# Kernel optimization log

Measured on AMD Instinct MI355X. Metric: run time of the kernel, lower is better.

## Reference

```python
import jax, jax.numpy as jnp
import numpy as np

T, N, H, L, V, B, MAX_NB = 32, 1024, 256, 128, 800, 256, 15
E = T * N  # total messages; buffer row E is the zero-pad slot


def setup_inputs() -> dict:
    key = jax.random.key(0)
    ks = jax.random.split(key, 12)

    def lin(k, o, i):
        return jax.random.normal(k, (o, i), jnp.float32) / np.float32(np.sqrt(i))

    rng = np.random.default_rng(0)
    # neighbor message indices: at step t only messages produced at steps < t are valid
    h_nei_idx = rng.integers(0, E, size=(T, N, MAX_NB))
    o_nei_idx = rng.integers(0, E, size=(T, N, MAX_NB))
    limit = (np.arange(T) * N)[:, None, None]
    h_nei_idx = np.where(h_nei_idx < limit, h_nei_idx, E)
    o_nei_idx = np.where(o_nei_idx < limit, o_nei_idx, E)

    return dict(
        emb=jax.random.normal(ks[0], (V, H), jnp.float32) * 0.02,
        W_z_w=lin(ks[1], H, 2 * H), W_z_b=jnp.zeros((H,), jnp.float32),
        W_r_w=lin(ks[2], H, H), W_r_b=jnp.zeros((H,), jnp.float32),
        U_r_w=lin(ks[3], H, H),
        W_h_w=lin(ks[4], H, 2 * H), W_h_b=jnp.zeros((H,), jnp.float32),
        W_w=lin(ks[5], H, H + L), W_b=jnp.zeros((H,), jnp.float32),
        Wo_w=lin(ks[6], V, H), Wo_b=jnp.zeros((V,), jnp.float32),
        U_w=lin(ks[7], H, H + L), U_b=jnp.zeros((H,), jnp.float32),
        Ui_w=lin(ks[8], H, 2 * H), Ui_b=jnp.zeros((H,), jnp.float32),
        Uo_w=lin(ks[9], 1, H), Uo_b=jnp.zeros((1,), jnp.float32),
        x_tree_vecs=jax.random.normal(ks[10], (B, L), jnp.float32),
        word_ids=jnp.asarray(rng.integers(0, V, size=(T, N)), jnp.int32),
        h_nei_idx=jnp.asarray(h_nei_idx, jnp.int32),
        o_nei_idx=jnp.asarray(o_nei_idx, jnp.int32),
        contexts=jnp.asarray(rng.integers(0, B, size=(T, N)), jnp.int32),
        pred_targets=jnp.asarray(rng.integers(0, V, size=(T, N)), jnp.int32),
        direction=jnp.asarray(rng.integers(0, 2, size=(T, N)), jnp.int32),
        root_word_ids=jnp.asarray(rng.integers(0, V, size=(B,)), jnp.int32),
        root_o_idx=jnp.asarray(rng.integers(0, E + 1, size=(B, MAX_NB)), jnp.int32),
    )


def reference(emb, W_z_w, W_z_b, W_r_w, W_r_b, U_r_w, W_h_w, W_h_b,
              W_w, W_b, Wo_w, Wo_b, U_w, U_b, Ui_w, Ui_b, Uo_w, Uo_b,
              x_tree_vecs, word_ids, h_nei_idx, o_nei_idx, contexts,
              pred_targets, direction, root_word_ids, root_o_idx):
    f32 = jnp.float32

    def gru(x, h_nei):  # x: [N,H], h_nei: [N,MAX_NB,H]
        sum_h = h_nei.sum(1)
        z = jax.nn.sigmoid(jnp.concatenate([x, sum_h], -1) @ W_z_w.T + W_z_b)
        r = jax.nn.sigmoid((x @ W_r_w.T + W_r_b)[:, None, :] + h_nei @ U_r_w.T)
        gated = (r * h_nei).sum(1)
        h_tilde = jnp.tanh(jnp.concatenate([x, gated], -1) @ W_h_w.T + W_h_b)
        return (1.0 - z) * sum_h + z * h_tilde

    def step(hbuf, xs):
        t, wid, hidx, oidx = xs
        x = emb[wid]                      # [N,H] embedding gather
        new_h = gru(x, hbuf[hidx])        # gather -> GRU
        cur_o = hbuf[oidx].sum(1)         # padded neighbor sum for stop head
        hbuf = jax.lax.dynamic_update_slice(hbuf, new_h, (t * N, 0))  # scatter
        return hbuf, (new_h, jnp.concatenate([x, cur_o], -1))

    hbuf0 = jnp.zeros((E + 1, H), f32)
    hbuf, (new_h_all, stop_h_all) = jax.lax.scan(
        step, hbuf0, (jnp.arange(T), word_ids, h_nei_idx, o_nei_idx))

    def aggregate(hid, ctx, Vw, Vb, Vow, Vob):
        iv = jnp.concatenate([hid, x_tree_vecs[ctx]], -1)
        return jax.nn.relu(iv @ Vw.T + Vb) @ Vow.T + Vob

    # ---- word prediction head: root entries (zero hidden) + direction==1 edges
    pred_hid = jnp.concatenate([jnp.zeros((B, H), f32), new_h_all.reshape(E, H)], 0)
    pred_ctx = jnp.concatenate([jnp.arange(B, dtype=jnp.int32), contexts.reshape(E)], 0)
    pred_tgt = jnp.concatenate([root_word_ids, pred_targets.reshape(E)], 0)
    pred_mask = jnp.concatenate([jnp.ones((B,), f32), direction.reshape(E).astype(f32)], 0)
    scores = aggregate(pred_hid, pred_ctx, W_w, W_b, Wo_w, Wo_b)  # [B+E, V]
    nll = -jnp.take_along_axis(jax.nn.log_softmax(scores, -1), pred_tgt[:, None], 1)[:, 0]
    pred_loss = (nll * pred_mask).sum() / B
    pred_acc = ((scores.argmax(-1) == pred_tgt).astype(f32) * pred_mask).sum() / pred_mask.sum()

    # ---- stop head: all edges + root closing entries
    root_stop = jnp.concatenate([emb[root_word_ids], hbuf[root_o_idx].sum(1)], -1)
    stop_hid = jnp.concatenate([stop_h_all.reshape(E, 2 * H), root_stop], 0)
    stop_ctx = jnp.concatenate([contexts.reshape(E), jnp.arange(B, dtype=jnp.int32)], 0)
    stop_tgt = jnp.concatenate([direction.reshape(E).astype(f32), jnp.zeros((B,), f32)], 0)
    stop_hid = jax.nn.relu(stop_hid @ Ui_w.T + Ui_b)  # U_i with relu
    s = aggregate(stop_hid, stop_ctx, U_w, U_b, Uo_w, Uo_b)[:, 0]
    bce = jnp.maximum(s, 0.0) - s * stop_tgt + jnp.log1p(jnp.exp(-jnp.abs(s)))
    stop_loss = bce.sum() / B
    stop_acc = ((s >= 0.0).astype(f32) == stop_tgt).astype(f32).mean()

    return pred_loss, stop_loss, pred_acc, stop_acc
```

## Files before the change

### kernel.cpp

```cpp
#include <hip/hip_runtime.h>
#include <math.h>


namespace {

constexpr int T_  = 32;
constexpr int N_  = 1024;
constexpr int H_  = 256;
constexpr int NB_ = 15;
constexpr int E_  = T_ * N_;
constexpr int B_  = 256;
constexpr int PREDB_ = (B_ + E_) / 64;
constexpr int STOPB_ = (E_ + B_) / 64;

typedef unsigned short u16;
typedef unsigned int   u32;
typedef unsigned int  uix4  __attribute__((ext_vector_type(4)));
typedef __bf16        bf16x8 __attribute__((ext_vector_type(8)));
typedef float         f32x4  __attribute__((ext_vector_type(4)));

__device__ __forceinline__ float sig_(float x){ return 1.f / (1.f + __expf(-x)); }

__device__ __forceinline__ float b2f(u16 u){
  union { u32 i; float f; } v; v.i = ((u32)u) << 16; return v.f;
}
__device__ __forceinline__ u16 f2b(float f){
  union { float f; u32 i; } v; v.f = f;
  const u32 r = v.i + 0x7fffu + ((v.i >> 16) & 1u);
  return (u16)(r >> 16);
}
__device__ __forceinline__ f32x4 mfma16(uix4 a, uix4 b, f32x4 c){
  return __builtin_amdgcn_mfma_f32_16x16x32_bf16(
      __builtin_bit_cast(bf16x8, a), __builtin_bit_cast(bf16x8, b), c, 0, 0, 0);
}

__global__ __launch_bounds__(256) void k_cvt(
    const float* __restrict__ emb, const float* __restrict__ xt,
    const float* __restrict__ Ww,  const float* __restrict__ Wo,
    const float* __restrict__ Ui,  const float* __restrict__ Uw,
    const float* __restrict__ Wz,  const float* __restrict__ Wr,
    const float* __restrict__ Ur,  const float* __restrict__ Wh,
    u16* __restrict__ o_emb, u16* __restrict__ o_xt, u16* __restrict__ o_Ww,
    u16* __restrict__ o_Wo,  u16* __restrict__ o_Ui, u16* __restrict__ o_Uw,
    u16* __restrict__ o_Wz,  u16* __restrict__ o_Wr, u16* __restrict__ o_Ur,
    u16* __restrict__ o_Wh)
{
  int i = blockIdx.x * 256 + threadIdx.x;
  if (i < 204800){ o_emb[i] = f2b(emb[i]); return; }  i -= 204800;
  if (i <  32768){ o_xt[i]  = f2b(xt[i]);  return; }  i -=  32768;
  if (i <  98304){ o_Ww[i]  = f2b(Ww[i]);  return; }  i -=  98304;
  if (i < 204800){ o_Wo[i]  = f2b(Wo[i]);  return; }  i -= 204800;
  if (i < 131072){ o_Ui[i]  = f2b(Ui[i]);  return; }  i -= 131072;
  if (i <  98304){ o_Uw[i]  = f2b(Uw[i]);  return; }  i -=  98304;
  if (i < 131072){ o_Wz[i]  = f2b(Wz[i]);  return; }  i -= 131072;
  if (i <  65536){ o_Wr[i]  = f2b(Wr[i]);  return; }  i -=  65536;
  if (i <  65536){ o_Ur[i]  = f2b(Ur[i]);  return; }  i -=  65536;
  if (i < 131072){ o_Wh[i]  = f2b(Wh[i]); }
}

__global__ __launch_bounds__(256) void k_rep(
    const u16* __restrict__ Ur16, const u16* __restrict__ Wz16,
    const u16* __restrict__ Wh16, const u16* __restrict__ Ui16,
    u16* __restrict__ UrF, u16* __restrict__ WzF, u16* __restrict__ WhF,
    u16* __restrict__ UiF)
{
  const int idx = blockIdx.x * 256 + threadIdx.x;
  if (idx < 24576){
    const int mat = idx >> 13, r = idx & 8191;
    const int ctkb = r >> 6, lane = r & 63;
    const int ct = ctkb >> 3, kb = ctkb & 7;
    const int q = lane >> 4, m = lane & 15;
    const int col = ct * 16 + m;
    const u16* src;
    u16* dst;
    if (mat == 0){ src = Ur16 + (size_t)col*256 +       kb*32 + q*8; dst = UrF; }
    else if (mat == 1){ src = Wz16 + (size_t)col*512 + 256 + kb*32 + q*8; dst = WzF; }
    else { src = Wh16 + (size_t)col*512 + 256 + kb*32 + q*8; dst = WhF; }
    *(uix4*)(dst + (size_t)r * 8) = *(const uix4*)src;
  } else {
    const int r = idx - 24576;
    if (r >= 16384) return;
    const int ctkb = r >> 6, lane = r & 63;
    const int ct = ctkb >> 4, kb = ctkb & 15;
    const int q = lane >> 4, m = lane & 15;
    const int col = ct * 16 + m;
    *(uix4*)(UiF + (size_t)r * 8) =
        *(const uix4*)(Ui16 + (size_t)col*512 + kb*32 + q*8);
  }
}

__global__ __launch_bounds__(256) void k_init(float* __restrict__ acc,
                                              u16* __restrict__ hb16){
  const int tid = threadIdx.x;
  if (tid < 16) acc[tid] = 0.f;
  hb16[(size_t)E_ * H_ + tid] = 0;
}

__global__ __launch_bounds__(256) void k_tab(
    const u16* __restrict__ emb16,
    const u16* __restrict__ Wr16, const float* __restrict__ Wrb,
    const u16* __restrict__ Wz16, const float* __restrict__ Wzb,
    const u16* __restrict__ Wh16, const float* __restrict__ Whb,
    float* __restrict__ xrtab, float* __restrict__ xztab,
    float* __restrict__ xhtab)
{
  const int tid = threadIdx.x;
  const int w = tid >> 6, ln = tid & 63, q = ln >> 4, m = ln & 15;
  const int r0 = blockIdx.x * 16;

  uix4 Ae[8];
  {
    const u16* ep = emb16 + (size_t)(r0 + m) * 256 + q * 8;
    #pragma unroll
    for (int kb = 0; kb < 8; ++kb) Ae[kb] = *(const uix4*)(ep + kb * 32);
  }
  #pragma unroll
  for (int nt = 0; nt < 4; ++nt){
    const int col = w * 64 + nt * 16 + m;
    f32x4 ar = {0.f,0.f,0.f,0.f}, az = {0.f,0.f,0.f,0.f}, ah = {0.f,0.f,0.f,0.f};
    const u16* br = Wr16 + (size_t)col * 256 + q * 8;
    const u16* bz = Wz16 + (size_t)col * 512 + q * 8;
    const u16* bh = Wh16 + (size_t)col * 512 + q * 8;
    #pragma unroll
    for (int kb = 0; kb < 8; ++kb){
      ar = mfma16(Ae[kb], *(const uix4*)(br + kb*32), ar);
      az = mfma16(Ae[kb], *(const uix4*)(bz + kb*32), az);
      ah = mfma16(Ae[kb], *(const uix4*)(bh + kb*32), ah);
    }
    const float rb = Wrb[col], zb = Wzb[col], hb = Whb[col];
    #pragma unroll
    for (int i = 0; i < 4; ++i){
      const size_t o = (size_t)(r0 + 4*q + i) * 256 + col;
      xrtab[o] = ar[i] + rb;
      xztab[o] = az[i] + zb;
      xhtab[o] = ah[i] + hb;
    }
  }
}

__global__ __launch_bounds__(1024, 4) void k_gru(
    const u16* __restrict__ UrF, const u16* __restrict__ WzF,
    const u16* __restrict__ WhF,
    const float* __restrict__ xrtab, const float* __restrict__ xztab,
    const float* __restrict__ xhtab,
    const int* __restrict__ word_ids, const int* __restrict__ h_nei,
    u16* __restrict__ hb16, int t)
{
  __shared__ __align__(16) u16 hn[64 * 264];
  __shared__ __align__(16) u16 sh[4][264];
  __shared__ __align__(16) u16 gl[4][264];
  __shared__ int s_wid[4];
  __shared__ int s_hidx[64];

  const int tid = threadIdx.x;
  const int w = tid >> 6, ln = tid & 63, q = ln >> 4, m = ln & 15;
  const int col  = w * 16 + m;
  const int base = t * N_ + blockIdx.x * 4;

  if (tid < 4) s_wid[tid] = word_ids[base + tid];
  if (tid < 64){
    const int row = tid & 3, nb = tid >> 2;
    s_hidx[tid] = (nb < NB_) ? h_nei[(base + row) * NB_ + nb] : E_;
  }

  const u16* urb = UrF + (size_t)(w * 8) * 512 + ln * 8;
  uix4 b0 = *(const uix4*)(urb);
  uix4 b1 = *(const uix4*)(urb + 512);
  uix4 b2 = *(const uix4*)(urb + 1024);
  uix4 b3 = *(const uix4*)(urb + 1536);
  uix4 b4 = *(const uix4*)(urb + 2048);
  uix4 b5 = *(const uix4*)(urb + 2560);
  uix4 b6 = *(const uix4*)(urb + 3072);
  uix4 b7 = *(const uix4*)(urb + 3584);

  __syncthreads();

  #pragma unroll
  for (int it = 0; it < 2; ++it){
    const int task = it * 1024 + tid;
    const int row = task >> 5, ch = task & 31;
    *(uix4*)(&hn[row*264 + ch*8]) =
        *(const uix4*)(hb16 + (size_t)s_hidx[row]*256 + ch*8);
  }
  __syncthreads();

  f32x4 xr;
  #pragma unroll
  for (int i = 0; i < 4; ++i) xr[i] = xrtab[(size_t)s_wid[i] * 256 + col];

  float ga[4] = {0.f,0.f,0.f,0.f}, su[4] = {0.f,0.f,0.f,0.f};
  #pragma unroll
  for (int j = 0; j < 4; ++j){
    uix4 Ah[8];
    #pragma unroll
    for (int kb = 0; kb < 8; ++kb)
      Ah[kb] = *(const uix4*)(&hn[(j*16 + m)*264 + kb*32 + q*8]);
    f32x4 a = xr;
    a = mfma16(Ah[0], b0, a); a = mfma16(Ah[1], b1, a);
    a = mfma16(Ah[2], b2, a); a = mfma16(Ah[3], b3, a);
    a = mfma16(Ah[4], b4, a); a = mfma16(Ah[5], b5, a);
    a = mfma16(Ah[6], b6, a); a = mfma16(Ah[7], b7, a);
    #pragma unroll
    for (int i = 0; i < 4; ++i){
      const float hv = b2f(hn[(j*16 + 4*q + i)*264 + col]);
      ga[i] += sig_(a[i]) * hv;
      su[i] += hv;
    }
  }

  #pragma unroll
  for (int i = 0; i < 4; ++i){
    ga[i] += __shfl_xor(ga[i], 16, 64);
    ga[i] += __shfl_xor(ga[i], 32, 64);
    su[i] += __shfl_xor(su[i], 16, 64);
    su[i] += __shfl_xor(su[i], 32, 64);
  }
  if (q == 0){
    #pragma unroll
    for (int i = 0; i < 4; ++i){
      sh[i][col] = f2b(su[i]);
      gl[i][col] = f2b(ga[i]);
    }
  }
  __syncthreads();

  f32x4 az, ah;
  #pragma unroll
  for (int i = 0; i < 4; ++i){
    az[i] = xztab[(size_t)s_wid[i] * 256 + col];
    ah[i] = xhtab[(size_t)s_wid[i] * 256 + col];
  }
  {
    const u16* zb = WzF + (size_t)(w * 8) * 512 + ln * 8;
    uix4 Bz[8];
    #pragma unroll
    for (int kb = 0; kb < 8; ++kb) Bz[kb] = *(const uix4*)(zb + kb * 512);
    uix4 As[8];
    #pragma unroll
    for (int kb = 0; kb < 8; ++kb) As[kb] = *(const uix4*)(&sh[m & 3][kb*32 + q*8]);
    #pragma unroll
    for (int kb = 0; kb < 8; ++kb) az = mfma16(As[kb], Bz[kb], az);
  }
  {
    const u16* hb = WhF + (size_t)(w * 8) * 512 + ln * 8;
    uix4 Bh[8];
    #pragma unroll
    for (int kb = 0; kb < 8; ++kb) Bh[kb] = *(const uix4*)(hb + kb * 512);
    uix4 Ag[8];
    #pragma unroll
    for (int kb = 0; kb < 8; ++kb) Ag[kb] = *(const uix4*)(&gl[m & 3][kb*32 + q*8]);
    #pragma unroll
    for (int kb = 0; kb < 8; ++kb) ah = mfma16(Ag[kb], Bh[kb], ah);
  }
  if (q == 0){
    #pragma unroll
    for (int i = 0; i < 4; ++i){
      const float z  = sig_(az[i]);
      const float ht = tanhf(ah[i]);
      const float nh = (1.f - z) * su[i] + z * ht;
      hb16[(size_t)(base + i) * 256 + col] = f2b(nh);
    }
  }
}

struct PredSm {
  u16   hd[4][16][264];
  u16   bt[32 * 264];
  int   tgt[64];
  float mask[64];
  float nll[64], hit[64], msk[64];
};
struct StopSm {
  u16   so[64][264];
  u16   bt[16 * 392];
  int   oidx[64][NB_];
  int   wid[64], ctx[64];
  float tgt[64];
  float b0[64], b1[64];
};
constexpr size_t SMU_ = sizeof(StopSm) > sizeof(PredSm) ? sizeof(StopSm)
                                                        : sizeof(PredSm);

__device__ void pred_body(int bid, char* smraw,
    const u16* __restrict__ hb16, const u16* __restrict__ Ww16,
    const float* __restrict__ Wb, const u16* __restrict__ Wo16,
    const float* __restrict__ Wob, const u16* __restrict__ xt16,
    const int* __restrict__ contexts, const int* __restrict__ pred_targets,
    const int* __restrict__ direction, const int* __restrict__ root_word_ids,
    float* __restrict__ accum)
{
  PredSm& sm = *(PredSm*)smraw;
  const int tid = threadIdx.x;
  const int p0  = bid * 64;
  const int w = tid >> 6, ln = tid & 63, q = ln >> 4, m = ln & 15;
  const int r0 = w * 16;

  if (tid < 64){
    const int p = p0 + tid;
    int tg; float mk;
    if (p < B_){ tg = root_word_ids[p]; mk = 1.f; }
    else { tg = pred_targets[p - B_]; mk = (float)direction[p - B_]; }
    sm.tgt[tid] = tg; sm.mask[tid] = mk;
  }
  const int p    = p0 + r0 + m;
  const int hrow = (p < B_) ? E_ : (p - B_);
  const int ctx  = (p < B_) ? p  : contexts[p - B_];

  uix4 A1[12];
  {
    const u16* hp = hb16 + (size_t)hrow * 256 + q * 8;
    #pragma unroll
    for (int j = 0; j < 8; ++j) A1[j] = *(const uix4*)(hp + j * 32);
    const u16* xp = xt16 + (size_t)ctx * 128 + q * 8;
    #pragma unroll
    for (int j = 0; j < 4; ++j) A1[8 + j] = *(const uix4*)(xp + j * 32);
  }

  {
    #pragma unroll
    for (int j = 0; j < 3; ++j){
      const int i = j*256 + tid, r = i / 48, c = i % 48;
      *(uix4*)(&sm.bt[r*392 + c*8]) = *(const uix4*)(Ww16 + (size_t)i*8);
    }
  }
  __syncthreads();
  for (int t = 0; t < 16; ++t){
    uix4 pf[3];
    if (t < 15){
      const u16* src = Ww16 + (size_t)(t+1)*16*384;
      #pragma unroll
      for (int j = 0; j < 3; ++j)
        pf[j] = *(const uix4*)(src + (size_t)(j*256 + tid)*8);
    }
    f32x4 acc = {0.f, 0.f, 0.f, 0.f};
    const u16* bp = &sm.bt[m*392 + q*8];
    #pragma unroll
    for (int j = 0; j < 12; ++j) acc = mfma16(A1[j], *(const uix4*)(bp + j*32), acc);
    const float bias = Wb[t*16 + m];
    #pragma unroll
    for (int i = 0; i < 4; ++i)
      sm.hd[w][q*4 + i][t*16 + m] = f2b(fmaxf(acc[i] + bias, 0.f));
    __syncthreads();
    if (t < 15){
      #pragma unroll
      for (int j = 0; j < 3; ++j){
        const int i = j*256 + tid, r = i / 48, c = i % 48;
        *(uix4*)(&sm.bt[r*392 + c*8]) = pf[j];
      }
      __syncthreads();
    }
  }

  uix4 A2[8];
  #pragma unroll
  for (int j = 0; j < 8; ++j) A2[j] = *(const uix4*)(&sm.hd[w][m][j*32 + q*8]);

  int tgtc[4];
  #pragma unroll
  for (int i = 0; i < 4; ++i) tgtc[i] = sm.tgt[r0 + q*4 + i];
  float lrun[4], amax[4], tval[4]; int aidx[4];
  #pragma unroll
  for (int i = 0; i < 4; ++i){
    lrun[i] = 0.f; amax[i] = -1e30f; tval[i] = -1e30f; aidx[i] = 0;
  }

  {
    #pragma unroll
    for (int j = 0; j < 4; ++j){
      const int i = j*256 + tid, r = i >> 5, c = i & 31;
      *(uix4*)(&sm.bt[r*264 + c*8]) = *(const uix4*)(Wo16 + (size_t)i*8);
    }
  }
  __syncthreads();
  for (int pp = 0; pp < 25; ++pp){
    uix4 pf[4];
    if (pp < 24){
      const u16* src = Wo16 + (size_t)(pp+1)*32*256;
      #pragma unroll
      for (int j = 0; j < 4; ++j)
        pf[j] = *(const uix4*)(src + (size_t)(j*256 + tid)*8);
    }
    f32x4 a0 = {0.f,0.f,0.f,0.f}, a1 = {0.f,0.f,0.f,0.f};
    const u16* bp0 = &sm.bt[m*264 + q*8];
    const u16* bp1 = &sm.bt[(16 + m)*264 + q*8];
    #pragma unroll
    for (int j = 0; j < 8; ++j){
      a0 = mfma16(A2[j], *(const uix4*)(bp0 + j*32), a0);
      a1 = mfma16(A2[j], *(const uix4*)(bp1 + j*32), a1);
    }
    const int c0 = pp*32 + m, c1 = c0 + 16;
    const float bias0 = Wob[c0], bias1 = Wob[c1];
    #pragma unroll
    for (int i = 0; i < 4; ++i){
      const float v0 = a0[i] + bias0;
      const float v1 = a1[i] + bias1;
      if (c0 == tgtc[i]) tval[i] = v0;
      if (c1 == tgtc[i]) tval[i] = v1;
      if (v0 > amax[i]){ amax[i] = v0; aidx[i] = c0; }
      if (v1 > amax[i]){ amax[i] = v1; aidx[i] = c1; }
      lrun[i] += __expf(v0) + __expf(v1);
    }
    __syncthreads();
    if (pp < 24){
      #pragma unroll
      for (int j = 0; j < 4; ++j){
        const int i = j*256 + tid, r = i >> 5, cc = i & 31;
        *(uix4*)(&sm.bt[r*264 + cc*8]) = pf[j];
      }
      __syncthreads();
    }
  }
  #pragma unroll
  for (int msk = 1; msk < 16; msk <<= 1){
    #pragma unroll
    for (int i = 0; i < 4; ++i){
      lrun[i] += __shfl_xor(lrun[i], msk, 64);
      const float oa = __shfl_xor(amax[i], msk, 64);
      const int   oi = __shfl_xor(aidx[i], msk, 64);
      if (oa > amax[i] || (oa == amax[i] && oi < aidx[i])){ amax[i] = oa; aidx[i] = oi; }
      tval[i] = fmaxf(tval[i], __shfl_xor(tval[i], msk, 64));
    }
  }
  if (m == 0){
    #pragma unroll
    for (int i = 0; i < 4; ++i){
      const int r = r0 + q*4 + i;
      const float mk  = sm.mask[r];
      const float nll = __logf(lrun[i]) - tval[i];
      sm.nll[r] = nll * mk;
      sm.hit[r] = (aidx[i] == tgtc[i]) ? mk : 0.f;
      sm.msk[r] = mk;
    }
  }
  __syncthreads();
  if (tid < 64){
    float a = sm.nll[tid], b = sm.hit[tid], c2 = sm.msk[tid];
    #pragma unroll
    for (int off = 32; off > 0; off >>= 1){
      a += __shfl_down(a, off, 64); b += __shfl_down(b, off, 64); c2 += __shfl_down(c2, off, 64);
    }
    if (tid == 0){
      atomicAdd(&accum[0], a); atomicAdd(&accum[1], b); atomicAdd(&accum[2], c2);
    }
  }
}

__device__ void stop_body(int bid, char* smraw,
    const u16* __restrict__ hb16, const u16* __restrict__ emb16,
    const u16* __restrict__ UiF,  const float* __restrict__ Uib,
    const u16* __restrict__ Uw16, const float* __restrict__ Ub,
    const float* __restrict__ Uo, const float* __restrict__ Uob,
    const u16* __restrict__ xt16,
    const int* __restrict__ word_ids, const int* __restrict__ o_nei,
    const int* __restrict__ contexts, const int* __restrict__ direction,
    const int* __restrict__ root_word_ids, const int* __restrict__ root_o_idx,
    float* __restrict__ accum)
{
  StopSm& sm = *(StopSm*)smraw;
  const int tid = threadIdx.x;
  const int p0  = bid * 64;
  const int w = tid >> 6, ln = tid & 63, q = ln >> 4, m = ln & 15;
  const int r0 = w * 16;

  if (tid < 64){
    const int s = p0 + tid;
    if (s < E_){ sm.wid[tid] = word_ids[s]; sm.ctx[tid] = contexts[s];
                 sm.tgt[tid] = (float)direction[s]; }
    else { const int b = s - E_; sm.wid[tid] = root_word_ids[b]; sm.ctx[tid] = b;
           sm.tgt[tid] = 0.f; }
  }
  for (int k = tid; k < 64 * NB_; k += 256){
    const int r = k / NB_, nb = k % NB_;
    const int s = p0 + r;
    sm.oidx[r][nb] = (s < E_) ? o_nei[(size_t)s * NB_ + nb]
                              : root_o_idx[(size_t)(s - E_) * NB_ + nb];
  }
  __syncthreads();

  for (int it = 0; it < 4; ++it){
    const int task = it * 256 + tid;
    const int row = task >> 4, sl = task & 15;
    float a[16];
    #pragma unroll
    for (int c = 0; c < 16; ++c) a[c] = 0.f;
    #pragma unroll
    for (int nb = 0; nb < NB_; ++nb){
      const u16* p = hb16 + (size_t)sm.oidx[row][nb] * 256 + sl * 16;
      const uix4 v0 = *(const uix4*)(p);
      const uix4 v1 = *(const uix4*)(p + 8);
      #pragma unroll
      for (int c = 0; c < 4; ++c){
        a[2*c]     += b2f((u16)(v0[c] & 0xffffu));
        a[2*c + 1] += b2f((u16)(v0[c] >> 16));
        a[8 + 2*c] += b2f((u16)(v1[c] & 0xffffu));
        a[9 + 2*c] += b2f((u16)(v1[c] >> 16));
      }
    }
    uix4 o0, o1;
    #pragma unroll
    for (int c = 0; c < 4; ++c){
      o0[c] = (u32)f2b(a[2*c])   | ((u32)f2b(a[2*c+1]) << 16);
      o1[c] = (u32)f2b(a[8+2*c]) | ((u32)f2b(a[9+2*c]) << 16);
    }
    *(uix4*)(&sm.so[row][sl*16])     = o0;
    *(uix4*)(&sm.so[row][sl*16 + 8]) = o1;
  }
  __syncthreads();

  uix4 A1[16];
  {
    const u16* ep = emb16 + (size_t)sm.wid[r0 + m] * 256 + q * 8;
    #pragma unroll
    for (int j = 0; j < 8; ++j) A1[j] = *(const uix4*)(ep + j * 32);
    #pragma unroll
    for (int j = 0; j < 8; ++j) A1[8 + j] = *(const uix4*)(&sm.so[r0 + m][j*32 + q*8]);
  }
  __syncthreads();

  for (int t = 0; t < 16; ++t){
    const u16* bp = UiF + (size_t)(t * 16) * 512 + ln * 8;
    uix4 Bf[16];
    #pragma unroll
    for (int kb = 0; kb < 16; ++kb) Bf[kb] = *(const uix4*)(bp + kb * 512);
    f32x4 acc = {0.f, 0.f, 0.f, 0.f};
    #pragma unroll
    for (int kb = 0; kb < 16; ++kb) acc = mfma16(A1[kb], Bf[kb], acc);
    const float bias = Uib[t*16 + m];
    #pragma unroll
    for (int i = 0; i < 4; ++i)
      sm.so[r0 + q*4 + i][t*16 + m] = f2b(fmaxf(acc[i] + bias, 0.f));
  }
  __syncthreads();

  uix4 A2[12];
  {
    #pragma unroll
    for (int j = 0; j < 8; ++j) A2[j] = *(const uix4*)(&sm.so[r0 + m][j*32 + q*8]);
    const u16* xp = xt16 + (size_t)sm.ctx[r0 + m] * 128 + q * 8;
    #pragma unroll
    for (int j = 0; j < 4; ++j) A2[8 + j] = *(const uix4*)(xp + j * 32);
  }
  float sp[4] = {0.f, 0.f, 0.f, 0.f};
  {
    #pragma unroll
    for (int j = 0; j < 3; ++j){
      const int i = j*256 + tid, r = i / 48, c = i % 48;
      *(uix4*)(&sm.bt[r*392 + c*8]) = *(const uix4*)(Uw16 + (size_t)i*8);
    }
  }
  __syncthreads();
  for (int t = 0; t < 16; ++t){
    uix4 pf[3];
    if (t < 15){
      const u16* src = Uw16 + (size_t)(t+1)*16*384;
      #pragma unroll
      for (int j = 0; j < 3; ++j)
        pf[j] = *(const uix4*)(src + (size_t)(j*256 + tid)*8);
    }
    f32x4 acc = {0.f, 0.f, 0.f, 0.f};
    const u16* bp = &sm.bt[m*392 + q*8];
    #pragma unroll
    for (int j = 0; j < 12; ++j) acc = mfma16(A2[j], *(const uix4*)(bp + j*32), acc);
    const int c = t*16 + m;
    const float bias = Ub[c];
    const float uo   = Uo[c];
    #pragma unroll
    for (int i = 0; i < 4; ++i) sp[i] += fmaxf(acc[i] + bias, 0.f) * uo;
    __syncthreads();
    if (t < 15){
      #pragma unroll
      for (int j = 0; j < 3; ++j){
        const int i = j*256 + tid, r = i / 48, cc = i % 48;
        *(uix4*)(&sm.bt[r*392 + cc*8]) = pf[j];
      }
      __syncthreads();
    }
  }
  #pragma unroll
  for (int msk = 1; msk < 16; msk <<= 1){
    #pragma unroll
    for (int i = 0; i < 4; ++i) sp[i] += __shfl_xor(sp[i], msk, 64);
  }
  if (m == 0){
    const float ub = Uob[0];
    #pragma unroll
    for (int i = 0; i < 4; ++i){
      const int r = r0 + q*4 + i;
      const float s   = sp[i] + ub;
      const float tgt = sm.tgt[r];
      sm.b0[r] = fmaxf(s, 0.f) - s * tgt + log1pf(__expf(-fabsf(s)));
      const float pb = (s >= 0.f) ? 1.f : 0.f;
      sm.b1[r] = (pb == tgt) ? 1.f : 0.f;
    }
  }
  __syncthreads();
  if (tid < 64){
    float a = sm.b0[tid], b = sm.b1[tid];
    #pragma unroll
    for (int off = 32; off > 0; off >>= 1){
      a += __shfl_down(a, off, 64); b += __shfl_down(b, off, 64);
    }
    if (tid == 0){ atomicAdd(&accum[3], a); atomicAdd(&accum[4], b); }
  }
}

__global__ __launch_bounds__(256, 3) void k_heads(
    const u16* __restrict__ hb16, const u16* __restrict__ emb16,
    const u16* __restrict__ Ww16, const float* __restrict__ Wb,
    const u16* __restrict__ Wo16, const float* __restrict__ Wob,
    const u16* __restrict__ UiF,  const float* __restrict__ Uib,
    const u16* __restrict__ Uw16, const float* __restrict__ Ub,
    const float* __restrict__ Uo, const float* __restrict__ Uob,
    const u16* __restrict__ xt16,
    const int* __restrict__ word_ids, const int* __restrict__ o_nei,
    const int* __restrict__ contexts, const int* __restrict__ pred_targets,
    const int* __restrict__ direction, const int* __restrict__ root_word_ids,
    const int* __restrict__ root_o_idx, float* __restrict__ accum)
{
  __shared__ __align__(16) char smraw[SMU_];
  const int b = blockIdx.x;
  if (b < PREDB_){
    pred_body(b, smraw, hb16, Ww16, Wb, Wo16, Wob, xt16,
              contexts, pred_targets, direction, root_word_ids, accum);
  } else {
    stop_body(b - PREDB_, smraw, hb16, emb16, UiF, Uib, Uw16, Ub, Uo, Uob,
              xt16, word_ids, o_nei, contexts, direction,
              root_word_ids, root_o_idx, accum);
  }
}

__global__ void k_final(const float* __restrict__ acc, float* __restrict__ out){
  if (threadIdx.x == 0 && blockIdx.x == 0){
    out[0] = acc[0] / (float)B_;
    out[1] = acc[3] / (float)B_;
    out[2] = acc[1] / acc[2];
    out[3] = acc[4] / (float)(E_ + B_);
  }
}

}

extern "C" void kernel_launch(void* const* d_in, const int* in_sizes, int n_in,
                              void* d_out, int out_size, void* d_ws, size_t ws_size,
                              hipStream_t stream)
{
  const float* emb   = (const float*)d_in[0];
  const float* Wz    = (const float*)d_in[1];
  const float* Wzb   = (const float*)d_in[2];
  const float* Wr    = (const float*)d_in[3];
  const float* Wrb   = (const float*)d_in[4];
  const float* Ur    = (const float*)d_in[5];
  const float* Wh    = (const float*)d_in[6];
  const float* Whb   = (const float*)d_in[7];
  const float* Ww    = (const float*)d_in[8];
  const float* Wb    = (const float*)d_in[9];
  const float* Wo    = (const float*)d_in[10];
  const float* Wob   = (const float*)d_in[11];
  const float* Uw    = (const float*)d_in[12];
  const float* Ub    = (const float*)d_in[13];
  const float* Ui    = (const float*)d_in[14];
  const float* Uib   = (const float*)d_in[15];
  const float* Uo    = (const float*)d_in[16];
  const float* Uob   = (const float*)d_in[17];
  const float* xtree = (const float*)d_in[18];
  const int* word_ids      = (const int*)d_in[19];
  const int* h_nei_idx     = (const int*)d_in[20];
  const int* o_nei_idx     = (const int*)d_in[21];
  const int* contexts      = (const int*)d_in[22];
  const int* pred_targets  = (const int*)d_in[23];
  const int* direction     = (const int*)d_in[24];
  const int* root_word_ids = (const int*)d_in[25];
  const int* root_o_idx    = (const int*)d_in[26];

  char*  wsb   = (char*)d_ws;
  float* accum = (float*)wsb;
  size_t off = 256 + 4096;
  u16* hb16  = (u16*)(wsb + off); off += (size_t)(E_ + 1) * H_ * 2;
  u16* emb16 = (u16*)(wsb + off); off += 204800u * 2;
  u16* xt16  = (u16*)(wsb + off); off += 32768u * 2;
  u16* Ww16  = (u16*)(wsb + off); off += 98304u * 2;
  u16* Wo16  = (u16*)(wsb + off); off += 204800u * 2;
  u16* Ui16  = (u16*)(wsb + off); off += 131072u * 2;
  u16* Uw16  = (u16*)(wsb + off); off += 98304u * 2;
  u16* Wz16  = (u16*)(wsb + off); off += 131072u * 2;
  u16* Wr16  = (u16*)(wsb + off); off += 65536u * 2;
  u16* Ur16  = (u16*)(wsb + off); off += 65536u * 2;
  u16* Wh16  = (u16*)(wsb + off); off += 131072u * 2;
  u16* UrF   = (u16*)(wsb + off); off += 65536u * 2;
  u16* WzF   = (u16*)(wsb + off); off += 65536u * 2;
  u16* WhF   = (u16*)(wsb + off); off += 65536u * 2;
  u16* UiF   = (u16*)(wsb + off); off += 131072u * 2;
  float* xrtab = (float*)(wsb + off); off += 204800u * 4;
  float* xztab = (float*)(wsb + off); off += 204800u * 4;
  float* xhtab = (float*)(wsb + off); off += 204800u * 4;
  float* out = (float*)d_out;

  hipLaunchKernelGGL(k_cvt, dim3(4544), dim3(256), 0, stream,
                     emb, xtree, Ww, Wo, Ui, Uw, Wz, Wr, Ur, Wh,
                     emb16, xt16, Ww16, Wo16, Ui16, Uw16,
                     Wz16, Wr16, Ur16, Wh16);
  hipLaunchKernelGGL(k_init, dim3(1), dim3(256), 0, stream, accum, hb16);
  hipLaunchKernelGGL(k_rep, dim3(160), dim3(256), 0, stream,
                     Ur16, Wz16, Wh16, Ui16, UrF, WzF, WhF, UiF);
  hipLaunchKernelGGL(k_tab, dim3(50), dim3(256), 0, stream,
                     emb16, Wr16, Wrb, Wz16, Wzb, Wh16, Whb,
                     xrtab, xztab, xhtab);

  for (int t = 0; t < T_; ++t){
    hipLaunchKernelGGL(k_gru, dim3(N_ / 4), dim3(1024), 0, stream,
                       UrF, WzF, WhF, xrtab, xztab, xhtab,
                       word_ids, h_nei_idx, hb16, t);
  }

  hipLaunchKernelGGL(k_heads, dim3(PREDB_ + STOPB_), dim3(256), 0, stream,
                     hb16, emb16, Ww16, Wb, Wo16, Wob, UiF, Uib, Uw16, Ub,
                     Uo, Uob, xt16, word_ids, o_nei_idx, contexts,
                     pred_targets, direction, root_word_ids, root_o_idx,
                     accum);

  hipLaunchKernelGGL(k_final, dim3(1), dim3(1), 0, stream, accum, out);
}
```

Measured before the change: 578.8 us.

## Double-buffer weight tiles in heads and drop shared index staging in GRU

In the pred and stop head kernels, the streamed weight tile now alternates between two shared buffers, reusing the hd and so regions once their contents have been loaded into registers. This removes one of the two block barriers per tile iteration. The GRU kernel stops staging word and neighbour indices in shared memory and reads them straight from global memory, removing one barrier. The cost is redundant global index loads per thread and reliance on the reused regions being dead before the overwrite.

```diff
diff --git a/kernel.cpp b/kernel.cpp
--- a/kernel.cpp
+++ b/kernel.cpp
@@ -149,19 +149,11 @@
   __shared__ __align__(16) u16 hn[64 * 264];
   __shared__ __align__(16) u16 sh[4][264];
   __shared__ __align__(16) u16 gl[4][264];
-  __shared__ int s_wid[4];
-  __shared__ int s_hidx[64];
 
   const int tid = threadIdx.x;
   const int w = tid >> 6, ln = tid & 63, q = ln >> 4, m = ln & 15;
   const int col  = w * 16 + m;
   const int base = t * N_ + blockIdx.x * 4;
-
-  if (tid < 4) s_wid[tid] = word_ids[base + tid];
-  if (tid < 64){
-    const int row = tid & 3, nb = tid >> 2;
-    s_hidx[tid] = (nb < NB_) ? h_nei[(base + row) * NB_ + nb] : E_;
-  }
 
   const u16* urb = UrF + (size_t)(w * 8) * 512 + ln * 8;
   uix4 b0 = *(const uix4*)(urb);
@@ -173,20 +165,20 @@
   uix4 b6 = *(const uix4*)(urb + 3072);
   uix4 b7 = *(const uix4*)(urb + 3584);
 
-  __syncthreads();
-
   #pragma unroll
   for (int it = 0; it < 2; ++it){
     const int task = it * 1024 + tid;
-    const int row = task >> 5, ch = task & 31;
-    *(uix4*)(&hn[row*264 + ch*8]) =
-        *(const uix4*)(hb16 + (size_t)s_hidx[row]*256 + ch*8);
+    const int p = task >> 5, ch = task & 31;
+    const int nb = p >> 2, row = p & 3;
+    const int idx = (nb < NB_) ? h_nei[(base + row) * NB_ + nb] : E_;
+    *(uix4*)(&hn[p*264 + ch*8]) =
+        *(const uix4*)(hb16 + (size_t)idx*256 + ch*8);
   }
   __syncthreads();
 
   f32x4 xr;
   #pragma unroll
-  for (int i = 0; i < 4; ++i) xr[i] = xrtab[(size_t)s_wid[i] * 256 + col];
+  for (int i = 0; i < 4; ++i) xr[i] = xrtab[(size_t)word_ids[base + i] * 256 + col];
 
   float ga[4] = {0.f,0.f,0.f,0.f}, su[4] = {0.f,0.f,0.f,0.f};
   #pragma unroll
@@ -227,8 +219,9 @@
   f32x4 az, ah;
   #pragma unroll
   for (int i = 0; i < 4; ++i){
-    az[i] = xztab[(size_t)s_wid[i] * 256 + col];
-    ah[i] = xhtab[(size_t)s_wid[i] * 256 + col];
+    const int wid = word_ids[base + i];
+    az[i] = xztab[(size_t)wid * 256 + col];
+    ah[i] = xhtab[(size_t)wid * 256 + col];
   }
   {
     const u16* zb = WzF + (size_t)(w * 8) * 512 + ln * 8;
@@ -364,15 +357,19 @@
     lrun[i] = 0.f; amax[i] = -1e30f; tval[i] = -1e30f; aidx[i] = 0;
   }
 
+  u16* g2buf0 = sm.bt;
+  u16* g2buf1 = &sm.hd[0][0][0];
   {
     #pragma unroll
     for (int j = 0; j < 4; ++j){
       const int i = j*256 + tid, r = i >> 5, c = i & 31;
-      *(uix4*)(&sm.bt[r*264 + c*8]) = *(const uix4*)(Wo16 + (size_t)i*8);
+      *(uix4*)(&g2buf0[r*264 + c*8]) = *(const uix4*)(Wo16 + (size_t)i*8);
     }
   }
   __syncthreads();
   for (int pp = 0; pp < 25; ++pp){
+    u16* cur = (pp & 1) ? g2buf1 : g2buf0;
+    u16* nxt = (pp & 1) ? g2buf0 : g2buf1;
     uix4 pf[4];
     if (pp < 24){
       const u16* src = Wo16 + (size_t)(pp+1)*32*256;
@@ -381,8 +378,8 @@
         pf[j] = *(const uix4*)(src + (size_t)(j*256 + tid)*8);
     }
     f32x4 a0 = {0.f,0.f,0.f,0.f}, a1 = {0.f,0.f,0.f,0.f};
-    const u16* bp0 = &sm.bt[m*264 + q*8];
-    const u16* bp1 = &sm.bt[(16 + m)*264 + q*8];
+    const u16* bp0 = cur + m*264 + q*8;
+    const u16* bp1 = cur + (16 + m)*264 + q*8;
     #pragma unroll
     for (int j = 0; j < 8; ++j){
       a0 = mfma16(A2[j], *(const uix4*)(bp0 + j*32), a0);
@@ -400,15 +397,14 @@
       if (v1 > amax[i]){ amax[i] = v1; aidx[i] = c1; }
       lrun[i] += __expf(v0) + __expf(v1);
     }
-    __syncthreads();
     if (pp < 24){
       #pragma unroll
       for (int j = 0; j < 4; ++j){
         const int i = j*256 + tid, r = i >> 5, cc = i & 31;
-        *(uix4*)(&sm.bt[r*264 + cc*8]) = pf[j];
+        *(uix4*)(&nxt[r*264 + cc*8]) = pf[j];
       }
-      __syncthreads();
-    }
+    }
+    __syncthreads();
   }
   #pragma unroll
   for (int msk = 1; msk < 16; msk <<= 1){
@@ -541,15 +537,19 @@
     for (int j = 0; j < 4; ++j) A2[8 + j] = *(const uix4*)(xp + j * 32);
   }
   float sp[4] = {0.f, 0.f, 0.f, 0.f};
+  u16* s2buf0 = sm.bt;
+  u16* s2buf1 = &sm.so[0][0];
   {
     #pragma unroll
     for (int j = 0; j < 3; ++j){
       const int i = j*256 + tid, r = i / 48, c = i % 48;
-      *(uix4*)(&sm.bt[r*392 + c*8]) = *(const uix4*)(Uw16 + (size_t)i*8);
+      *(uix4*)(&s2buf0[r*392 + c*8]) = *(const uix4*)(Uw16 + (size_t)i*8);
     }
   }
   __syncthreads();
   for (int t = 0; t < 16; ++t){
+    u16* cur = (t & 1) ? s2buf1 : s2buf0;
+    u16* nxt = (t & 1) ? s2buf0 : s2buf1;
     uix4 pf[3];
     if (t < 15){
       const u16* src = Uw16 + (size_t)(t+1)*16*384;
@@ -558,7 +558,7 @@
         pf[j] = *(const uix4*)(src + (size_t)(j*256 + tid)*8);
     }
     f32x4 acc = {0.f, 0.f, 0.f, 0.f};
-    const u16* bp = &sm.bt[m*392 + q*8];
+    const u16* bp = cur + m*392 + q*8;
     #pragma unroll
     for (int j = 0; j < 12; ++j) acc = mfma16(A2[j], *(const uix4*)(bp + j*32), acc);
     const int c = t*16 + m;
@@ -566,15 +566,14 @@
     const float uo   = Uo[c];
     #pragma unroll
     for (int i = 0; i < 4; ++i) sp[i] += fmaxf(acc[i] + bias, 0.f) * uo;
-    __syncthreads();
     if (t < 15){
       #pragma unroll
       for (int j = 0; j < 3; ++j){
         const int i = j*256 + tid, r = i / 48, cc = i % 48;
-        *(uix4*)(&sm.bt[r*392 + cc*8]) = pf[j];
+        *(uix4*)(&nxt[r*392 + cc*8]) = pf[j];
       }
-      __syncthreads();
-    }
+    }
+    __syncthreads();
   }
   #pragma unroll
   for (int msk = 1; msk < 16; msk <<= 1){
```

Result: no change. 582.5 us (+0.6%).
